# Performance work log

Measured on AMD Instinct MI355X. Metric: run time of the kernel, lower is better.

The kernel has to match this reference:

```python
import jax, jax.numpy as jnp
import numpy as np

B, S, D = 4, 4096, 128

def setup_inputs() -> dict:
    key = jax.random.key(0)
    ks = jax.random.split(key, 7)
    s = 1.0 / np.sqrt(D)
    return {
        "x": jax.random.normal(ks[0], (B, S, D), dtype=jnp.float32),
        "Wq": jax.random.normal(ks[1], (D, D), dtype=jnp.float32) * s,
        "bq": jax.random.normal(ks[2], (D,), dtype=jnp.float32) * s,
        "Wk": jax.random.normal(ks[3], (D, D), dtype=jnp.float32) * s,
        "bk": jax.random.normal(ks[4], (D,), dtype=jnp.float32) * s,
        "Wv": jax.random.normal(ks[5], (D, D), dtype=jnp.float32) * s,
        "bv": jax.random.normal(ks[6], (D,), dtype=jnp.float32) * s,
    }

def reference(x, Wq, bq, Wk, bk, Wv, bv):
    # Linear projections (torch Linear: x @ W^T + b)
    Q = jnp.einsum('bsd,ed->bse', x, Wq) + bq
    K = jnp.einsum('bsd,ed->bse', x, Wk) + bk
    V = jnp.einsum('bsd,ed->bse', x, Wv) + bv
    scale = jnp.sqrt(jnp.asarray(x.shape[-1], dtype=x.dtype))
    scores = jnp.einsum('bqd,bkd->bqk', Q, K) / scale  # [B,S,S]
    weights = jax.nn.softmax(scores, axis=-1)
    return jnp.einsum('bqk,bkd->bqd', weights, V)
```

## Files before the change

kernel.cpp:

```cpp
#include <hip/hip_runtime.h>
#include <hip/hip_bf16.h>
#include <stdint.h>

#define NB 4
#define NS 4096
#define ND 128
#define KVBLK 32
#define NT32 (NS / KVBLK)
#define QBLK 128

typedef __attribute__((ext_vector_type(8))) short short8;
typedef __attribute__((ext_vector_type(4))) float f32x4;
typedef __attribute__((ext_vector_type(16))) float f32x16;
typedef __attribute__((ext_vector_type(2))) int i32x2;
typedef _Float16 f16;

#define QSCALE 0.12751744f

__device__ __forceinline__ unsigned short f2bfu(float f) {
  __hip_bfloat16 h = __float2bfloat16(f);
  union { __hip_bfloat16 h; unsigned short u; } c; c.h = h; return c.u;
}
__device__ __forceinline__ uint32_t pack2bf(float lo, float hi) {
  return (uint32_t)f2bfu(lo) | ((uint32_t)f2bfu(hi) << 16);
}

__device__ __forceinline__ void gl_lds16(const void* g, void* l) {
  __builtin_amdgcn_global_load_lds(
      (const __attribute__((address_space(1))) uint32_t*)g,
      (__attribute__((address_space(3))) uint32_t*)l, 16, 0, 0);
}

#define MFMA16(a, b, c) __builtin_amdgcn_mfma_f32_16x16x32_bf16((a), (b), (c), 0, 0, 0)
#define MFMA32(a, b, c) __builtin_amdgcn_mfma_f32_32x32x16_bf16((a), (b), (c), 0, 0, 0)

#if __has_builtin(__builtin_amdgcn_permlane32_swap)
#define PLSWAP(lo_, hi_)                                                        \
  { i32x2 r_ = __builtin_amdgcn_permlane32_swap((int)(lo_), (int)(hi_), false,  \
                                                false);                         \
    lo_ = (uint32_t)r_[0]; hi_ = (uint32_t)r_[1]; }
#else
#define PLSWAP(lo_, hi_)                                                        \
  { uint32_t sA_ = hi ? (lo_) : (hi_);                                          \
    uint32_t rA_ = (uint32_t)__shfl_xor((int)sA_, 32, 64);                      \
    uint32_t nl_ = hi ? rA_ : (lo_);                                            \
    uint32_t nh_ = hi ? (hi_) : rA_;                                            \
    lo_ = nl_; hi_ = nh_; }
#endif

__global__ __launch_bounds__(512) void preconv_kernel(
    const float* __restrict__ x,
    const float* __restrict__ Wq, const float* __restrict__ Wk,
    const float* __restrict__ Wv,
    unsigned short* __restrict__ xb, unsigned short* __restrict__ Wb)
{
  const size_t xg8 = (size_t)NB * NS * ND / 8;
  size_t i = (size_t)blockIdx.x * 512 + threadIdx.x;
  const float* src; unsigned short* dst; size_t off;
  if (i < xg8) { src = x; dst = xb; off = i * 8; }
  else {
    size_t j = i - xg8;
    int which = (int)(j / 2048);
    src = which == 0 ? Wq : which == 1 ? Wk : Wv;
    dst = Wb;
    off = j * 8;
    src = src - (size_t)which * 16384;
  }
  float4 a = *(const float4*)(src + off), b2 = *(const float4*)(src + off + 4);
  short8 o;
  o[0] = (short)f2bfu(a.x);  o[1] = (short)f2bfu(a.y);
  o[2] = (short)f2bfu(a.z);  o[3] = (short)f2bfu(a.w);
  o[4] = (short)f2bfu(b2.x); o[5] = (short)f2bfu(b2.y);
  o[6] = (short)f2bfu(b2.z); o[7] = (short)f2bfu(b2.w);
  *(short8*)(dst + off) = o;
}

__global__ __launch_bounds__(256) void proj_kernel(
    const unsigned short* __restrict__ xb, const unsigned short* __restrict__ Wb,
    const float* __restrict__ bq, const float* __restrict__ bk,
    const float* __restrict__ bv,
    unsigned short* __restrict__ Qo, unsigned short* __restrict__ Ko,
    unsigned short* __restrict__ Vt)
{
  __shared__ unsigned short Xs[64 * 128];
  __shared__ unsigned short Ws[128 * 128];

  const int tile = blockIdx.x, b = blockIdx.y, which = blockIdx.z;
  const float* bias = which == 0 ? bq : which == 1 ? bk : bv;
  const int t = threadIdx.x, wave = t >> 6, lane = t & 63;
  const int lr = lane & 15, lg = lane >> 4;

  const char* xsrc = (const char*)(xb + ((size_t)b * NS + (size_t)tile * 64) * ND);
#pragma unroll
  for (int i = wave; i < 16; i += 4) {
    int y = i * 1024 + lane * 16;
    int so = y ^ (((y >> 8) & 7) << 4);
    gl_lds16(xsrc + so, (char*)Xs + y);
  }
  const char* wsrc = (const char*)(Wb + (size_t)which * 16384);
#pragma unroll
  for (int i = wave; i < 32; i += 4) {
    int y = i * 1024 + lane * 16;
    int so = y ^ (((y >> 8) & 7) << 4);
    gl_lds16(wsrc + so, (char*)Ws + y);
  }
  __syncthreads();

  short8 af[4];
#pragma unroll
  for (int kk = 0; kk < 4; ++kk) {
    int row = wave * 16 + lr;
    int ba = (row * 256 + kk * 64 + lg * 16) ^ ((row & 7) << 4);
    af[kk] = *(const short8*)((const char*)Xs + ba);
  }
  f32x4 acc[8] = {};
#pragma unroll
  for (int kk = 0; kk < 4; ++kk) {
#pragma unroll
    for (int nf = 0; nf < 8; ++nf) {
      int n = nf * 16 + lr;
      int ba = (n * 256 + kk * 64 + lg * 16) ^ ((n & 7) << 4);
      short8 bf = *(const short8*)((const char*)Ws + ba);
      acc[nf] = MFMA16(af[kk], bf, acc[nf]);
    }
  }

  if (which < 2) {
    unsigned short* Out = (which == 0) ? Qo : Ko;
    const float sc = (which == 0) ? QSCALE : 1.0f;
#pragma unroll
    for (int nf = 0; nf < 8; ++nf) {
      float bb = bias[nf * 16 + lr];
#pragma unroll
      for (int r = 0; r < 4; ++r) {
        float v = (acc[nf][r] + bb) * sc;
        int row = tile * 64 + wave * 16 + lg * 4 + r;
        Out[((size_t)b * NS + row) * ND + nf * 16 + lr] = f2bfu(v);
      }
    }
  } else {
    __syncthreads();
    unsigned short* Tt = Ws;
#pragma unroll
    for (int nf = 0; nf < 8; ++nf) {
      float bb = bias[nf * 16 + lr];
#pragma unroll
      for (int r = 0; r < 4; ++r) {
        int e = nf * 16 + lr;
        int sl = wave * 16 + lg * 4 + r;
        Tt[e * 72 + sl] = f2bfu(acc[nf][r] + bb);
      }
    }
    __syncthreads();
    int e = t >> 1, off = (t & 1) * 32;
    const short8* src = (const short8*)(Tt + e * 72 + off);
    short8* dst = (short8*)(Vt + ((size_t)b * ND + e) * NS + (size_t)tile * 64 + off);
#pragma unroll
    for (int i = 0; i < 4; ++i) dst[i] = src[i];
  }
}

__global__ __launch_bounds__(256, 3) void attn_kernel(
    const unsigned short* __restrict__ Q, const unsigned short* __restrict__ K,
    const unsigned short* __restrict__ Vt, f16* __restrict__ OP,
    float* __restrict__ Mp, float* __restrict__ Lp, int nchunk)
{
  __shared__ char smem[32768];

  const int Lid = blockIdx.x;
  const int ngroups = NB * nchunk;
  int g, qt;
  if ((ngroups & 7) == 0) {
    int xcd = Lid & 7, s2 = Lid >> 3;
    qt = s2 & 31;
    g = xcd * (ngroups >> 3) + (s2 >> 5);
  } else { qt = Lid & 31; g = Lid >> 5; }
  const int b = g / nchunk, c = g - b * nchunk;

  const int cbase = NT32 / nchunk, crem = NT32 - cbase * nchunk;
  const int tstart = c * cbase + (c < crem ? c : crem);
  const int ntpc = cbase + (c < crem ? 1 : 0);

  const int t = threadIdx.x, wave = t >> 6, lane = t & 63;
  const int lq = lane & 31, hi = lane >> 5;

  const int qrow = qt * QBLK + wave * 32 + lq;
  short8 qf[8];
  const unsigned short* Qb = Q + ((size_t)b * NS + qrow) * ND;
#pragma unroll
  for (int kt = 0; kt < 8; ++kt) qf[kt] = *(const short8*)(Qb + kt * 16 + hi * 8);

  const char* Kbase = (const char*)(K + (size_t)b * NS * ND) +
                      (size_t)tstart * (KVBLK * ND * 2);
  const char* Vbase = (const char*)(Vt + (size_t)b * ND * NS) +
                      (size_t)tstart * (KVBLK * 2);

  auto stage = [&](int p, int tt) {
    const char* ksrc = Kbase + (size_t)tt * 8192;
    const char* vsrc = Vbase + (size_t)tt * 64;
    char* kd = smem + p * 8192;
    char* vd = smem + 16384 + p * 8192;
#pragma unroll
    for (int j = 0; j < 2; ++j) {
      int y = (wave * 2 + j) * 1024 + lane * 16;
      int so = y ^ (((y >> 8) & 15) << 4);
      gl_lds16(ksrc + so, kd + y);
      int d = y >> 6, col = y & 63;
      int cx = col ^ (((d >> 1) & 3) << 4);
      gl_lds16(vsrc + (size_t)d * (NS * 2) + cx, vd + y);
    }
  };

  f32x16 oacc[4] = {};
  float m = -1e30f, l = 0.f;

  stage(0, 0);
  __syncthreads();

  for (int tt = 0; tt < ntpc; ++tt) {
    const int p = tt & 1;
    const char* kb = smem + p * 8192;
    const char* vb = smem + 16384 + p * 8192;
    if (tt + 1 < ntpc) stage(p ^ 1, tt + 1);

    f32x16 s0 = {};
    const int ksw = (lq & 15) << 4;
    __builtin_amdgcn_s_setprio(1);
#pragma unroll
    for (int kt = 0; kt < 8; ++kt) {
      int co = (kt * 32 + hi * 16) ^ ksw;
      short8 k0 = *(const short8*)(kb + lq * 256 + co);
      s0 = MFMA32(k0, qf[kt], s0);
    }
    __builtin_amdgcn_s_setprio(0);

    float x0 = fmaxf(s0[0], s0[1]), x1 = fmaxf(s0[2], s0[3]);
    float x2 = fmaxf(s0[4], s0[5]), x3 = fmaxf(s0[6], s0[7]);
#pragma unroll
    for (int r = 8; r < 16; r += 4) {
      x0 = fmaxf(x0, s0[r]);     x1 = fmaxf(x1, s0[r + 1]);
      x2 = fmaxf(x2, s0[r + 2]); x3 = fmaxf(x3, s0[r + 3]);
    }
    float px = fmaxf(fmaxf(x0, x1), fmaxf(x2, x3));
    px = fmaxf(px, __shfl_xor(px, 32, 64));
    if (__any(px > m + 8.f)) {
      float mn = fmaxf(m, px);
      float corr = exp2f(m - mn);
      m = mn;
      l *= corr;
#pragma unroll
      for (int dt = 0; dt < 4; ++dt)
#pragma unroll
        for (int r = 0; r < 16; ++r) oacc[dt][r] *= corr;
    }

    float u0 = 0.f, u1 = 0.f, u2 = 0.f, u3 = 0.f;
#pragma unroll
    for (int r = 0; r < 16; r += 4) {
      s0[r]     = exp2f(s0[r] - m);
      s0[r + 1] = exp2f(s0[r + 1] - m);
      s0[r + 2] = exp2f(s0[r + 2] - m);
      s0[r + 3] = exp2f(s0[r + 3] - m);
      u0 += s0[r]; u1 += s0[r + 1]; u2 += s0[r + 2]; u3 += s0[r + 3];
    }
    l += (u0 + u1) + (u2 + u3);

    uint32_t pk[8];
#pragma unroll
    for (int i = 0; i < 8; ++i) pk[i] = pack2bf(s0[2 * i], s0[2 * i + 1]);
    short8 pfrag[2];
#pragma unroll
    for (int kt2 = 0; kt2 < 2; ++kt2) {
      uint32_t e0 = pk[4 * kt2 + 0], e1 = pk[4 * kt2 + 1];
      uint32_t e2 = pk[4 * kt2 + 2], e3 = pk[4 * kt2 + 3];
      PLSWAP(e0, e2);
      PLSWAP(e1, e3);
      union { uint32_t u[4]; short8 s; } pf;
      pf.u[0] = e0; pf.u[1] = e1; pf.u[2] = e2; pf.u[3] = e3;
      pfrag[kt2] = pf.s;
    }

    const int vsw = ((lq >> 1) & 3) << 4;
    __builtin_amdgcn_s_setprio(1);
#pragma unroll
    for (int dt = 0; dt < 4; ++dt) {
      int rowb = (dt * 32 + lq) * 64;
#pragma unroll
      for (int kt2 = 0; kt2 < 2; ++kt2) {
        int co = (kt2 * 32 + hi * 16) ^ vsw;
        short8 vf = *(const short8*)(vb + rowb + co);
        oacc[dt] = MFMA32(vf, pfrag[kt2], oacc[dt]);
      }
    }
    __builtin_amdgcn_s_setprio(0);

    __syncthreads();
  }

  float lt = l + __shfl_xor(l, 32, 64);
  f16* OPb = OP + ((size_t)(c * NB + b) * ND) * NS + qrow;
#pragma unroll
  for (int dt = 0; dt < 4; ++dt)
#pragma unroll
    for (int r = 0; r < 16; ++r) {
      int d = dt * 32 + (r & 3) + 8 * (r >> 2) + 4 * hi;
      OPb[(size_t)d * NS] = (f16)oacc[dt][r];
    }
  if (hi == 0) {
    Mp[(size_t)(c * NB + b) * NS + qrow] = m;
    Lp[(size_t)(c * NB + b) * NS + qrow] = lt;
  }
}

template <int NC>
__global__ __launch_bounds__(256) void combine_kernel(
    const f16* __restrict__ OP, const float* __restrict__ Mp,
    const float* __restrict__ Lp, float* __restrict__ Out)
{
  __shared__ float wn[NC][64];
  __shared__ float LT[64][129];

  const int qtile = blockIdx.x, b = blockIdx.y;
  const int t = threadIdx.x;

  if (t < 64) {
    size_t qg = (size_t)qtile * 64 + t;
    float mv[NC], wloc[NC];
#pragma unroll
    for (int cc = 0; cc < NC; ++cc)
      mv[cc] = Mp[(size_t)(cc * NB + b) * NS + qg];
    float mx = mv[0];
#pragma unroll
    for (int cc = 1; cc < NC; ++cc) mx = fmaxf(mx, mv[cc]);
    float Lt = 0.f;
#pragma unroll
    for (int cc = 0; cc < NC; ++cc) {
      float w = exp2f(mv[cc] - mx);
      Lt += w * Lp[(size_t)(cc * NB + b) * NS + qg];
      wloc[cc] = w;
    }
    float inv = 1.0f / Lt;
#pragma unroll
    for (int cc = 0; cc < NC; ++cc) wn[cc][t] = wloc[cc] * inv;
  }
  __syncthreads();

  const int so = (t & 7) * 8;
  const int dl = t >> 3;
  const size_t sbase = (size_t)qtile * 64 + so;
#pragma unroll
  for (int dblk = 0; dblk < 4; ++dblk) {
    int d = dblk * 32 + dl;
    float a0 = 0, a1 = 0, a2 = 0, a3 = 0, a4 = 0, a5 = 0, a6 = 0, a7 = 0;
#pragma unroll
    for (int cc = 0; cc < NC; ++cc) {
      const f16* src = OP + ((size_t)(cc * NB + b) * ND + d) * NS + sbase;
      short8 v = *(const short8*)src;
      const float* w = &wn[cc][so];
      union { short s; f16 h; } u;
      u.s = v[0]; a0 += w[0] * (float)u.h;
      u.s = v[1]; a1 += w[1] * (float)u.h;
      u.s = v[2]; a2 += w[2] * (float)u.h;
      u.s = v[3]; a3 += w[3] * (float)u.h;
      u.s = v[4]; a4 += w[4] * (float)u.h;
      u.s = v[5]; a5 += w[5] * (float)u.h;
      u.s = v[6]; a6 += w[6] * (float)u.h;
      u.s = v[7]; a7 += w[7] * (float)u.h;
    }
    LT[so + 0][d] = a0; LT[so + 1][d] = a1;
    LT[so + 2][d] = a2; LT[so + 3][d] = a3;
    LT[so + 4][d] = a4; LT[so + 5][d] = a5;
    LT[so + 6][d] = a6; LT[so + 7][d] = a7;
  }
  __syncthreads();

  const int d2 = t & 127, qh = t >> 7;
  float* Ob = Out + ((size_t)b * NS + (size_t)qtile * 64) * ND;
#pragma unroll 8
  for (int pass = 0; pass < 32; ++pass) {
    int qq = pass * 2 + qh;
    Ob[(size_t)qq * ND + d2] = LT[qq][d2];
  }
}

extern "C" void kernel_launch(void* const* d_in, const int* in_sizes, int n_in,
                              void* d_out, int out_size, void* d_ws, size_t ws_size,
                              hipStream_t stream) {
  const float* x  = (const float*)d_in[0];
  const float* Wq = (const float*)d_in[1];
  const float* bq = (const float*)d_in[2];
  const float* Wk = (const float*)d_in[3];
  const float* bk = (const float*)d_in[4];
  const float* Wv = (const float*)d_in[5];
  const float* bv = (const float*)d_in[6];

  const size_t elems = (size_t)NB * NS * ND;
  char* base = (char*)d_ws;
  unsigned short* Qw  = (unsigned short*)base;
  unsigned short* Kw  = Qw + elems;
  unsigned short* Vtw = Kw + elems;
  char* region2 = base + 3 * elems * 2;

  int nchunk = 6;
  for (;;) {
    size_t need = 3 * elems * 2 +
                  (size_t)nchunk * (elems * 2 + 2 * (size_t)NB * NS * 4);
    if (need <= ws_size || nchunk == 1) break;
    nchunk = (nchunk == 6) ? 4 : nchunk >> 1;
  }

  unsigned short* xb16 = (unsigned short*)region2;
  unsigned short* Wb16 = xb16 + elems;
  f16* OPw = (f16*)region2;
  float* Mpw = (float*)(region2 + (size_t)nchunk * elems * 2);
  float* Lpw = Mpw + (size_t)nchunk * NB * NS;

  preconv_kernel<<<dim3(524), 512, 0, stream>>>(x, Wq, Wk, Wv, xb16, Wb16);

  proj_kernel<<<dim3(NS / 64, NB, 3), 256, 0, stream>>>(
      xb16, Wb16, bq, bk, bv, Qw, Kw, Vtw);

  attn_kernel<<<dim3(32 * NB * nchunk), 256, 0, stream>>>(
      Qw, Kw, Vtw, OPw, Mpw, Lpw, nchunk);

  dim3 cgrid(NS / 64, NB);
  switch (nchunk) {
    case 6: combine_kernel<6><<<cgrid, 256, 0, stream>>>(OPw, Mpw, Lpw, (float*)d_out); break;
    case 4: combine_kernel<4><<<cgrid, 256, 0, stream>>>(OPw, Mpw, Lpw, (float*)d_out); break;
    case 2: combine_kernel<2><<<cgrid, 256, 0, stream>>>(OPw, Mpw, Lpw, (float*)d_out); break;
    default: combine_kernel<1><<<cgrid, 256, 0, stream>>>(OPw, Mpw, Lpw, (float*)d_out); break;
  }
}
```

Measured before the change: 75.08 us.

## Process two 32-row query tiles per wave to reuse K/V LDS fragments

Each wave now handles 64 query rows (two 32-row sub-tiles), so every K and V fragment read from LDS feeds two MFMAs instead of one. This halves LDS traffic and staging per query row, at the cost of doubled accumulator and Q-fragment registers, so launch bounds drop to 2 blocks per SIMD. The KV split count becomes a template parameter, the default changes from 6 to 8 chunks, and the grid is 512 blocks.

```diff
diff --git a/kernel.cpp b/kernel.cpp
--- a/kernel.cpp
+++ b/kernel.cpp
@@ -7,7 +7,7 @@
 #define ND 128
 #define KVBLK 32
 #define NT32 (NS / KVBLK)
-#define QBLK 128
+#define QBLK 256
 
 typedef __attribute__((ext_vector_type(8))) short short8;
 typedef __attribute__((ext_vector_type(4))) float f32x4;
@@ -160,35 +160,38 @@
   }
 }
 
-__global__ __launch_bounds__(256, 3) void attn_kernel(
+template <int NC>
+__global__ __launch_bounds__(256, 2) void attn_kernel(
     const unsigned short* __restrict__ Q, const unsigned short* __restrict__ K,
     const unsigned short* __restrict__ Vt, f16* __restrict__ OP,
-    float* __restrict__ Mp, float* __restrict__ Lp, int nchunk)
+    float* __restrict__ Mp, float* __restrict__ Lp)
 {
   __shared__ char smem[32768];
 
   const int Lid = blockIdx.x;
-  const int ngroups = NB * nchunk;
+  constexpr int ngroups = NB * NC;
   int g, qt;
-  if ((ngroups & 7) == 0) {
+  if constexpr ((ngroups & 7) == 0) {
     int xcd = Lid & 7, s2 = Lid >> 3;
-    qt = s2 & 31;
-    g = xcd * (ngroups >> 3) + (s2 >> 5);
-  } else { qt = Lid & 31; g = Lid >> 5; }
-  const int b = g / nchunk, c = g - b * nchunk;
-
-  const int cbase = NT32 / nchunk, crem = NT32 - cbase * nchunk;
-  const int tstart = c * cbase + (c < crem ? c : crem);
-  const int ntpc = cbase + (c < crem ? 1 : 0);
+    qt = s2 & 15;
+    g = xcd * (ngroups >> 3) + (s2 >> 4);
+  } else { qt = Lid & 15; g = Lid >> 4; }
+  const int b = g / NC, c = g - b * NC;
+
+  constexpr int ntpc = NT32 / NC;
+  const int tstart = c * ntpc;
 
   const int t = threadIdx.x, wave = t >> 6, lane = t & 63;
   const int lq = lane & 31, hi = lane >> 5;
 
-  const int qrow = qt * QBLK + wave * 32 + lq;
-  short8 qf[8];
-  const unsigned short* Qb = Q + ((size_t)b * NS + qrow) * ND;
-#pragma unroll
-  for (int kt = 0; kt < 8; ++kt) qf[kt] = *(const short8*)(Qb + kt * 16 + hi * 8);
+  const int qrowA = qt * QBLK + wave * 64 + lq;
+  short8 qfA[8], qfB[8];
+  const unsigned short* QbA = Q + ((size_t)b * NS + qrowA) * ND;
+#pragma unroll
+  for (int kt = 0; kt < 8; ++kt) {
+    qfA[kt] = *(const short8*)(QbA + kt * 16 + hi * 8);
+    qfB[kt] = *(const short8*)(QbA + 32 * ND + kt * 16 + hi * 8);
+  }
 
   const char* Kbase = (const char*)(K + (size_t)b * NS * ND) +
                       (size_t)tstart * (KVBLK * ND * 2);
@@ -211,35 +214,16 @@
     }
   };
 
-  f32x16 oacc[4] = {};
-  float m = -1e30f, l = 0.f;
-
-  stage(0, 0);
-  __syncthreads();
-
-  for (int tt = 0; tt < ntpc; ++tt) {
-    const int p = tt & 1;
-    const char* kb = smem + p * 8192;
-    const char* vb = smem + 16384 + p * 8192;
-    if (tt + 1 < ntpc) stage(p ^ 1, tt + 1);
-
-    f32x16 s0 = {};
-    const int ksw = (lq & 15) << 4;
-    __builtin_amdgcn_s_setprio(1);
-#pragma unroll
-    for (int kt = 0; kt < 8; ++kt) {
-      int co = (kt * 32 + hi * 16) ^ ksw;
-      short8 k0 = *(const short8*)(kb + lq * 256 + co);
-      s0 = MFMA32(k0, qf[kt], s0);
-    }
-    __builtin_amdgcn_s_setprio(0);
-
-    float x0 = fmaxf(s0[0], s0[1]), x1 = fmaxf(s0[2], s0[3]);
-    float x2 = fmaxf(s0[4], s0[5]), x3 = fmaxf(s0[6], s0[7]);
+  f32x16 oaccA[4] = {}, oaccB[4] = {};
+  float mA = -1e30f, lA = 0.f, mB = -1e30f, lB = 0.f;
+
+  auto smx = [&](f32x16& s, float& m, float& l, f32x16* oa, short8* pf) {
+    float x0 = fmaxf(s[0], s[1]), x1 = fmaxf(s[2], s[3]);
+    float x2 = fmaxf(s[4], s[5]), x3 = fmaxf(s[6], s[7]);
 #pragma unroll
     for (int r = 8; r < 16; r += 4) {
-      x0 = fmaxf(x0, s0[r]);     x1 = fmaxf(x1, s0[r + 1]);
-      x2 = fmaxf(x2, s0[r + 2]); x3 = fmaxf(x3, s0[r + 3]);
+      x0 = fmaxf(x0, s[r]);     x1 = fmaxf(x1, s[r + 1]);
+      x2 = fmaxf(x2, s[r + 2]); x3 = fmaxf(x3, s[r + 3]);
     }
     float px = fmaxf(fmaxf(x0, x1), fmaxf(x2, x3));
     px = fmaxf(px, __shfl_xor(px, 32, 64));
@@ -251,34 +235,57 @@
 #pragma unroll
       for (int dt = 0; dt < 4; ++dt)
 #pragma unroll
-        for (int r = 0; r < 16; ++r) oacc[dt][r] *= corr;
-    }
-
+        for (int r = 0; r < 16; ++r) oa[dt][r] *= corr;
+    }
     float u0 = 0.f, u1 = 0.f, u2 = 0.f, u3 = 0.f;
 #pragma unroll
     for (int r = 0; r < 16; r += 4) {
-      s0[r]     = exp2f(s0[r] - m);
-      s0[r + 1] = exp2f(s0[r + 1] - m);
-      s0[r + 2] = exp2f(s0[r + 2] - m);
-      s0[r + 3] = exp2f(s0[r + 3] - m);
-      u0 += s0[r]; u1 += s0[r + 1]; u2 += s0[r + 2]; u3 += s0[r + 3];
+      s[r]     = exp2f(s[r] - m);
+      s[r + 1] = exp2f(s[r + 1] - m);
+      s[r + 2] = exp2f(s[r + 2] - m);
+      s[r + 3] = exp2f(s[r + 3] - m);
+      u0 += s[r]; u1 += s[r + 1]; u2 += s[r + 2]; u3 += s[r + 3];
     }
     l += (u0 + u1) + (u2 + u3);
-
     uint32_t pk[8];
 #pragma unroll
-    for (int i = 0; i < 8; ++i) pk[i] = pack2bf(s0[2 * i], s0[2 * i + 1]);
-    short8 pfrag[2];
+    for (int i = 0; i < 8; ++i) pk[i] = pack2bf(s[2 * i], s[2 * i + 1]);
 #pragma unroll
     for (int kt2 = 0; kt2 < 2; ++kt2) {
       uint32_t e0 = pk[4 * kt2 + 0], e1 = pk[4 * kt2 + 1];
       uint32_t e2 = pk[4 * kt2 + 2], e3 = pk[4 * kt2 + 3];
       PLSWAP(e0, e2);
       PLSWAP(e1, e3);
-      union { uint32_t u[4]; short8 s; } pf;
-      pf.u[0] = e0; pf.u[1] = e1; pf.u[2] = e2; pf.u[3] = e3;
-      pfrag[kt2] = pf.s;
-    }
+      union { uint32_t u[4]; short8 s8; } w;
+      w.u[0] = e0; w.u[1] = e1; w.u[2] = e2; w.u[3] = e3;
+      pf[kt2] = w.s8;
+    }
+  };
+
+  stage(0, 0);
+  __syncthreads();
+
+  for (int tt = 0; tt < ntpc; ++tt) {
+    const int p = tt & 1;
+    const char* kb = smem + p * 8192;
+    const char* vb = smem + 16384 + p * 8192;
+    if (tt + 1 < ntpc) stage(p ^ 1, tt + 1);
+
+    f32x16 sA = {}, sB = {};
+    const int ksw = (lq & 15) << 4;
+    __builtin_amdgcn_s_setprio(1);
+#pragma unroll
+    for (int kt = 0; kt < 8; ++kt) {
+      int co = (kt * 32 + hi * 16) ^ ksw;
+      short8 k0 = *(const short8*)(kb + lq * 256 + co);
+      sA = MFMA32(k0, qfA[kt], sA);
+      sB = MFMA32(k0, qfB[kt], sB);
+    }
+    __builtin_amdgcn_s_setprio(0);
+
+    short8 pfA[2], pfB[2];
+    smx(sA, mA, lA, oaccA, pfA);
+    smx(sB, mB, lB, oaccB, pfB);
 
     const int vsw = ((lq >> 1) & 3) << 4;
     __builtin_amdgcn_s_setprio(1);
@@ -289,7 +296,8 @@
       for (int kt2 = 0; kt2 < 2; ++kt2) {
         int co = (kt2 * 32 + hi * 16) ^ vsw;
         short8 vf = *(const short8*)(vb + rowb + co);
-        oacc[dt] = MFMA32(vf, pfrag[kt2], oacc[dt]);
+        oaccA[dt] = MFMA32(vf, pfA[kt2], oaccA[dt]);
+        oaccB[dt] = MFMA32(vf, pfB[kt2], oaccB[dt]);
       }
     }
     __builtin_amdgcn_s_setprio(0);
@@ -297,18 +305,22 @@
     __syncthreads();
   }
 
-  float lt = l + __shfl_xor(l, 32, 64);
-  f16* OPb = OP + ((size_t)(c * NB + b) * ND) * NS + qrow;
+  float ltA = lA + __shfl_xor(lA, 32, 64);
+  float ltB = lB + __shfl_xor(lB, 32, 64);
+  f16* OPbA = OP + ((size_t)(c * NB + b) * ND) * NS + qrowA;
 #pragma unroll
   for (int dt = 0; dt < 4; ++dt)
 #pragma unroll
     for (int r = 0; r < 16; ++r) {
       int d = dt * 32 + (r & 3) + 8 * (r >> 2) + 4 * hi;
-      OPb[(size_t)d * NS] = (f16)oacc[dt][r];
+      OPbA[(size_t)d * NS] = (f16)oaccA[dt][r];
+      OPbA[(size_t)d * NS + 32] = (f16)oaccB[dt][r];
     }
   if (hi == 0) {
-    Mp[(size_t)(c * NB + b) * NS + qrow] = m;
-    Lp[(size_t)(c * NB + b) * NS + qrow] = lt;
+    Mp[(size_t)(c * NB + b) * NS + qrowA] = mA;
+    Lp[(size_t)(c * NB + b) * NS + qrowA] = ltA;
+    Mp[(size_t)(c * NB + b) * NS + qrowA + 32] = mB;
+    Lp[(size_t)(c * NB + b) * NS + qrowA + 32] = ltB;
   }
 }
 
@@ -401,12 +413,12 @@
   unsigned short* Vtw = Kw + elems;
   char* region2 = base + 3 * elems * 2;
 
-  int nchunk = 6;
-  for (;;) {
+  int nchunk = 8;
+  while (nchunk > 1) {
     size_t need = 3 * elems * 2 +
                   (size_t)nchunk * (elems * 2 + 2 * (size_t)NB * NS * 4);
-    if (need <= ws_size || nchunk == 1) break;
-    nchunk = (nchunk == 6) ? 4 : nchunk >> 1;
+    if (need <= ws_size) break;
+    nchunk >>= 1;
   }
 
   unsigned short* xb16 = (unsigned short*)region2;
@@ -420,14 +432,24 @@
   proj_kernel<<<dim3(NS / 64, NB, 3), 256, 0, stream>>>(
       xb16, Wb16, bq, bk, bv, Qw, Kw, Vtw);
 
-  attn_kernel<<<dim3(32 * NB * nchunk), 256, 0, stream>>>(
-      Qw, Kw, Vtw, OPw, Mpw, Lpw, nchunk);
-
+  float* out = (float*)d_out;
   dim3 cgrid(NS / 64, NB);
   switch (nchunk) {
-    case 6: combine_kernel<6><<<cgrid, 256, 0, stream>>>(OPw, Mpw, Lpw, (float*)d_out); break;
-    case 4: combine_kernel<4><<<cgrid, 256, 0, stream>>>(OPw, Mpw, Lpw, (float*)d_out); break;
-    case 2: combine_kernel<2><<<cgrid, 256, 0, stream>>>(OPw, Mpw, Lpw, (float*)d_out); break;
-    default: combine_kernel<1><<<cgrid, 256, 0, stream>>>(OPw, Mpw, Lpw, (float*)d_out); break;
-  }
-}
+    case 8:
+      attn_kernel<8><<<dim3(16 * NB * 8), 256, 0, stream>>>(Qw, Kw, Vtw, OPw, Mpw, Lpw);
+      combine_kernel<8><<<cgrid, 256, 0, stream>>>(OPw, Mpw, Lpw, out);
+      break;
+    case 4:
+      attn_kernel<4><<<dim3(16 * NB * 4), 256, 0, stream>>>(Qw, Kw, Vtw, OPw, Mpw, Lpw);
+      combine_kernel<4><<<cgrid, 256, 0, stream>>>(OPw, Mpw, Lpw, out);
+      break;
+    case 2:
+      attn_kernel<2><<<dim3(16 * NB * 2), 256, 0, stream>>>(Qw, Kw, Vtw, OPw, Mpw, Lpw);
+      combine_kernel<2><<<cgrid, 256, 0, stream>>>(OPw, Mpw, Lpw, out);
+      break;
+    default:
+      attn_kernel<1><<<dim3(16 * NB * 1), 256, 0, stream>>>(Qw, Kw, Vtw, OPw, Mpw, Lpw);
+      combine_kernel<1><<<cgrid, 256, 0, stream>>>(OPw, Mpw, Lpw, out);
+      break;
+  }
+}
```

Measured after the change: 79.93 us. 6.5% more time.

## Software-pipeline QK^T one tile ahead of softmax and PV in attention loop

Applied to the files above, without the earlier changes.

Splits K and V staging so K is prefetched two tiles ahead and V one tile ahead, and computes the next tile's QK^T scores before running softmax and PV on the current tile. The aim is to let the score MFMAs overlap with the exp/max VALU work and hide the dependency stall between QK^T and softmax. It also replaces the pairwise max reduction with three-input max calls. The cost is higher register pressure from holding two score tiles, and more complex buffer reuse timing between the K and V double buffers.

```diff
diff --git a/kernel.cpp b/kernel.cpp
--- a/kernel.cpp
+++ b/kernel.cpp
@@ -23,6 +23,9 @@
 }
 __device__ __forceinline__ uint32_t pack2bf(float lo, float hi) {
   return (uint32_t)f2bfu(lo) | ((uint32_t)f2bfu(hi) << 16);
+}
+__device__ __forceinline__ float fmax3(float a, float b, float c) {
+  return fmaxf(fmaxf(a, b), c);
 }
 
 __device__ __forceinline__ void gl_lds16(const void* g, void* l) {
@@ -195,53 +198,53 @@
   const char* Vbase = (const char*)(Vt + (size_t)b * ND * NS) +
                       (size_t)tstart * (KVBLK * 2);
 
-  auto stage = [&](int p, int tt) {
+  auto stageK = [&](int p, int tt) {
     const char* ksrc = Kbase + (size_t)tt * 8192;
-    const char* vsrc = Vbase + (size_t)tt * 64;
     char* kd = smem + p * 8192;
-    char* vd = smem + 16384 + p * 8192;
 #pragma unroll
     for (int j = 0; j < 2; ++j) {
       int y = (wave * 2 + j) * 1024 + lane * 16;
       int so = y ^ (((y >> 8) & 15) << 4);
       gl_lds16(ksrc + so, kd + y);
+    }
+  };
+  auto stageV = [&](int p, int tt) {
+    const char* vsrc = Vbase + (size_t)tt * 64;
+    char* vd = smem + 16384 + p * 8192;
+#pragma unroll
+    for (int j = 0; j < 2; ++j) {
+      int y = (wave * 2 + j) * 1024 + lane * 16;
       int d = y >> 6, col = y & 63;
       int cx = col ^ (((d >> 1) & 3) << 4);
       gl_lds16(vsrc + (size_t)d * (NS * 2) + cx, vd + y);
     }
   };
 
+  const int ksw = (lq & 15) << 4;
+  auto QK = [&](int p) {
+    f32x16 s = {};
+    const char* kbp = smem + p * 8192;
+    __builtin_amdgcn_s_setprio(1);
+#pragma unroll
+    for (int kt = 0; kt < 8; ++kt) {
+      int co = (kt * 32 + hi * 16) ^ ksw;
+      short8 k0 = *(const short8*)(kbp + lq * 256 + co);
+      s = MFMA32(k0, qf[kt], s);
+    }
+    __builtin_amdgcn_s_setprio(0);
+    return s;
+  };
+
   f32x16 oacc[4] = {};
   float m = -1e30f, l = 0.f;
 
-  stage(0, 0);
-  __syncthreads();
-
-  for (int tt = 0; tt < ntpc; ++tt) {
-    const int p = tt & 1;
-    const char* kb = smem + p * 8192;
-    const char* vb = smem + 16384 + p * 8192;
-    if (tt + 1 < ntpc) stage(p ^ 1, tt + 1);
-
-    f32x16 s0 = {};
-    const int ksw = (lq & 15) << 4;
-    __builtin_amdgcn_s_setprio(1);
-#pragma unroll
-    for (int kt = 0; kt < 8; ++kt) {
-      int co = (kt * 32 + hi * 16) ^ ksw;
-      short8 k0 = *(const short8*)(kb + lq * 256 + co);
-      s0 = MFMA32(k0, qf[kt], s0);
-    }
-    __builtin_amdgcn_s_setprio(0);
-
-    float x0 = fmaxf(s0[0], s0[1]), x1 = fmaxf(s0[2], s0[3]);
-    float x2 = fmaxf(s0[4], s0[5]), x3 = fmaxf(s0[6], s0[7]);
-#pragma unroll
-    for (int r = 8; r < 16; r += 4) {
-      x0 = fmaxf(x0, s0[r]);     x1 = fmaxf(x1, s0[r + 1]);
-      x2 = fmaxf(x2, s0[r + 2]); x3 = fmaxf(x3, s0[r + 3]);
-    }
-    float px = fmaxf(fmaxf(x0, x1), fmaxf(x2, x3));
+  auto smx = [&](f32x16& s, short8* pf) {
+    float x0 = fmax3(s[0], s[1], s[2]);
+    float x1 = fmax3(s[3], s[4], s[5]);
+    float x2 = fmax3(s[6], s[7], s[8]);
+    float x3 = fmax3(s[9], s[10], s[11]);
+    float x4 = fmax3(s[12], s[13], s[14]);
+    float px = fmaxf(fmax3(x0, x1, x2), fmax3(x3, x4, s[15]));
     px = fmaxf(px, __shfl_xor(px, 32, 64));
     if (__any(px > m + 8.f)) {
       float mn = fmaxf(m, px);
@@ -253,34 +256,51 @@
 #pragma unroll
         for (int r = 0; r < 16; ++r) oacc[dt][r] *= corr;
     }
-
     float u0 = 0.f, u1 = 0.f, u2 = 0.f, u3 = 0.f;
 #pragma unroll
     for (int r = 0; r < 16; r += 4) {
-      s0[r]     = exp2f(s0[r] - m);
-      s0[r + 1] = exp2f(s0[r + 1] - m);
-      s0[r + 2] = exp2f(s0[r + 2] - m);
-      s0[r + 3] = exp2f(s0[r + 3] - m);
-      u0 += s0[r]; u1 += s0[r + 1]; u2 += s0[r + 2]; u3 += s0[r + 3];
+      s[r]     = exp2f(s[r] - m);
+      s[r + 1] = exp2f(s[r + 1] - m);
+      s[r + 2] = exp2f(s[r + 2] - m);
+      s[r + 3] = exp2f(s[r + 3] - m);
+      u0 += s[r]; u1 += s[r + 1]; u2 += s[r + 2]; u3 += s[r + 3];
     }
     l += (u0 + u1) + (u2 + u3);
-
     uint32_t pk[8];
 #pragma unroll
-    for (int i = 0; i < 8; ++i) pk[i] = pack2bf(s0[2 * i], s0[2 * i + 1]);
-    short8 pfrag[2];
+    for (int i = 0; i < 8; ++i) pk[i] = pack2bf(s[2 * i], s[2 * i + 1]);
 #pragma unroll
     for (int kt2 = 0; kt2 < 2; ++kt2) {
       uint32_t e0 = pk[4 * kt2 + 0], e1 = pk[4 * kt2 + 1];
       uint32_t e2 = pk[4 * kt2 + 2], e3 = pk[4 * kt2 + 3];
       PLSWAP(e0, e2);
       PLSWAP(e1, e3);
-      union { uint32_t u[4]; short8 s; } pf;
-      pf.u[0] = e0; pf.u[1] = e1; pf.u[2] = e2; pf.u[3] = e3;
-      pfrag[kt2] = pf.s;
-    }
-
-    const int vsw = ((lq >> 1) & 3) << 4;
+      union { uint32_t u[4]; short8 s8; } w;
+      w.u[0] = e0; w.u[1] = e1; w.u[2] = e2; w.u[3] = e3;
+      pf[kt2] = w.s8;
+    }
+  };
+
+  stageK(0, 0);
+  stageV(0, 0);
+  if (ntpc > 1) stageK(1, 1);
+  __syncthreads();
+  f32x16 sC = QK(0);
+  __syncthreads();
+
+  const int vsw = ((lq >> 1) & 3) << 4;
+  for (int tt = 0; tt < ntpc; ++tt) {
+    const bool haveNext = (tt + 1 < ntpc);
+    if (tt + 2 < ntpc) stageK(tt & 1, tt + 2);
+    if (haveNext) stageV((tt + 1) & 1, tt + 1);
+
+    f32x16 sN;
+    if (haveNext) sN = QK((tt + 1) & 1);
+
+    short8 pf[2];
+    smx(sC, pf);
+
+    const char* vb = smem + 16384 + (tt & 1) * 8192;
     __builtin_amdgcn_s_setprio(1);
 #pragma unroll
     for (int dt = 0; dt < 4; ++dt) {
@@ -289,12 +309,13 @@
       for (int kt2 = 0; kt2 < 2; ++kt2) {
         int co = (kt2 * 32 + hi * 16) ^ vsw;
         short8 vf = *(const short8*)(vb + rowb + co);
-        oacc[dt] = MFMA32(vf, pfrag[kt2], oacc[dt]);
+        oacc[dt] = MFMA32(vf, pf[kt2], oacc[dt]);
       }
     }
     __builtin_amdgcn_s_setprio(0);
 
     __syncthreads();
+    if (haveNext) sC = sN;
   }
 
   float lt = l + __shfl_xor(l, 32, 64);
```

New measurement: 79.80 us. 6.3% more time.
